# Optimization experiments

Hardware: AMD Instinct MI355X
Metric: run time of the kernel (lower is better)

Reference implementation:

```python
import jax, jax.numpy as jnp
import numpy as np

ENS, N_UNITS, N_HID, IN_DIM, OUT_DIM, BATCH = 10, 256, 7, 6, 201, 16384


def setup_inputs() -> dict:
    key = jax.random.key(0)
    ks = jax.random.split(key, 8)
    # He/fan-in scaled weights so activations stay sane through 8 ReLU layers
    W0 = jax.random.normal(ks[0], (ENS, IN_DIM, N_UNITS), jnp.float32) / np.sqrt(IN_DIM)
    b0 = jax.random.normal(ks[1], (ENS, N_UNITS), jnp.float32) * 0.01
    Wh = jax.random.normal(ks[2], (N_HID, ENS, N_UNITS, N_UNITS), jnp.float32) / np.sqrt(N_UNITS)
    bh = jax.random.normal(ks[3], (N_HID, ENS, N_UNITS), jnp.float32) * 0.01
    Wf = jax.random.normal(ks[4], (ENS, N_UNITS, OUT_DIM), jnp.float32) / np.sqrt(N_UNITS)
    bf = jax.random.normal(ks[5], (ENS, OUT_DIM), jnp.float32) * 0.01
    x = jax.random.normal(ks[6], (BATCH, IN_DIM), jnp.float32)
    return {"x": x, "W0": W0, "b0": b0, "Wh": Wh, "bh": bh, "Wf": Wf, "bf": bf}


def reference(x, W0, b0, Wh, bh, Wf, bf):
    # Ensemble of MLPs (grouped 1x1 conv == per-ensemble dense layers).
    # Input is broadcast to every ensemble member (torch.cat tiling).
    h = jax.nn.relu(jnp.einsum('bi,eio->beo', x, W0) + b0)  # (B, ens, 256)

    def step(h, wb):
        W, b = wb
        return jax.nn.relu(jnp.einsum('beh,eho->beo', h, W) + b), None

    h, _ = jax.lax.scan(step, h, (Wh, bh))  # 7 hidden layers
    y = jnp.einsum('beh,eho->beo', h, Wf) + bf  # (B, ens, out_dim), ens-major channels
    B, E, O = y.shape
    # Faithful to torch: view(B, out_dim, ens_size) on ens-major flat channels,
    # then mean over last dim (mixes strided channel chunks, not true ensemble mean).
    return y.reshape(B, O, E).mean(axis=-1)  # (B, out_dim)
```

## Files before the change

### kernel.cpp

```cpp
#include <hip/hip_runtime.h>

typedef unsigned int u32;
typedef unsigned short ushort_t;

typedef __attribute__((ext_vector_type(8)))  short bf16x8;
typedef __attribute__((ext_vector_type(16))) float f32x16;

#define ENS 10
#define NU 256
#define NHID 7
#define IN_DIM 6
#define OUT_DIM 201
#define BATCH 16384


#define WH_PER 65536
#define WH_TOT (NHID * ENS * WH_PER)
#define W0_PER 4096
#define W0_TOT (ENS * W0_PER)
#define WF_PER 57344
#define WF_TOT (ENS * WF_PER)
#define X_TOT ((BATCH / 32) * 64 * 8)

#define O_WHH 0
#define O_WHL (O_WHH + WH_TOT)
#define O_W0H (O_WHL + WH_TOT)
#define O_W0L (O_W0H + W0_TOT)
#define O_WFH (O_W0L + W0_TOT)
#define O_WFL (O_WFH + WF_TOT)
#define O_XH  (O_WFL + WF_TOT)
#define O_XL  (O_XH + X_TOT)
#define O_P   (O_XL + X_TOT)

#define NG 21
#define RS 264
#define YS 204
#define RT 64

__device__ __forceinline__ u32 bf16_rne(float f) {
    u32 u = __float_as_uint(f);
    return (u + 0x7FFFu + ((u >> 16) & 1u)) >> 16;
}
__device__ __forceinline__ void split2(float f, u32& h, u32& l) {
    h = bf16_rne(f);
    float fh = __uint_as_float(h << 16);
    l = bf16_rne(f - fh);
}

__device__ __forceinline__ u32 cvt_pk_bf16(float s0, float s1) {
    u32 r;
    asm("v_cvt_pk_bf16_f32 %0, %1, %2" : "=v"(r) : "v"(s0), "v"(s1));
    return r;
}

#define GLOAD(dst, p) \
    asm volatile("global_load_dwordx4 %0, %1, off" : "=v"(dst) : "v"(p))
#define VMWAIT4 asm volatile("s_waitcnt vmcnt(4)" ::: "memory")
#define VMWAIT0 asm volatile("s_waitcnt vmcnt(0)" ::: "memory")


__global__ __launch_bounds__(256) void prep_wh(const float* __restrict__ Wh,
                                               ushort_t* __restrict__ dH, ushort_t* __restrict__ dL) {
    int i = blockIdx.x * 256 + threadIdx.x;
    if (i >= WH_TOT) return;
    int j = i & 7, l = (i >> 3) & 63, ctg = (i >> 9) & 7, s = (i >> 12) & 15, le = i >> 16;
    int k = s * 16 + ((l >> 5) << 3) + j;
    int n = ctg * 32 + (l & 31);
    float v = Wh[(size_t)le * 65536 + k * 256 + n];
    u32 h, lo; split2(v, h, lo);
    dH[i] = (ushort_t)h; dL[i] = (ushort_t)lo;
}

__global__ __launch_bounds__(256) void prep_w0(const float* __restrict__ W0,
                                               ushort_t* __restrict__ dH, ushort_t* __restrict__ dL) {
    int i = blockIdx.x * 256 + threadIdx.x;
    if (i >= W0_TOT) return;
    int j = i & 7, l = (i >> 3) & 63, ctg = (i >> 9) & 7, e = i >> 12;
    int k = ((l >> 5) << 3) + j;
    int n = ctg * 32 + (l & 31);
    float v = (k < IN_DIM) ? W0[(e * IN_DIM + k) * 256 + n] : 0.0f;
    u32 h, lo; split2(v, h, lo);
    dH[i] = (ushort_t)h; dL[i] = (ushort_t)lo;
}

__global__ __launch_bounds__(256) void prep_wf(const float* __restrict__ Wf,
                                               ushort_t* __restrict__ dH, ushort_t* __restrict__ dL) {
    int i = blockIdx.x * 256 + threadIdx.x;
    if (i >= WF_TOT) return;
    int e = i / WF_PER;
    int idx = i - e * WF_PER;
    int j = idx & 7, l = (idx >> 3) & 63, g = idx >> 9;
    int s = g / 7, ct = g - s * 7;
    int k = s * 16 + ((l >> 5) << 3) + j;
    int n = ct * 32 + (l & 31);
    float v = (n < OUT_DIM) ? Wf[((size_t)e * 256 + k) * OUT_DIM + n] : 0.0f;
    u32 h, lo; split2(v, h, lo);
    dH[i] = (ushort_t)h; dL[i] = (ushort_t)lo;
}

__global__ __launch_bounds__(256) void prep_x(const float* __restrict__ x,
                                              ushort_t* __restrict__ dH, ushort_t* __restrict__ dL) {
    int i = blockIdx.x * 256 + threadIdx.x;
    if (i >= X_TOT) return;
    int j = i & 7, l = (i >> 3) & 63, rt = i >> 9;
    int row = rt * 32 + (l & 31);
    int k = ((l >> 5) << 3) + j;
    float v = (k < IN_DIM) ? x[row * IN_DIM + k] : 0.0f;
    u32 h, lo; split2(v, h, lo);
    dH[i] = (ushort_t)h; dL[i] = (ushort_t)lo;
}

__global__ __launch_bounds__(256) void reduce_mean(const float* __restrict__ P,
                                                   float* __restrict__ out) {
    int i = blockIdx.x * 256 + threadIdx.x;
    if (i >= BATCH * OUT_DIM) return;
    int b = i / OUT_DIM, jo = i - b * OUT_DIM;
    int f0 = jo * 10;
    int e1 = f0 / OUT_DIM;
    int e2 = (f0 + 9) / OUT_DIM;
    int g1 = jo - (e1 * OUT_DIM) / 10;
    float s = P[((size_t)e1 * BATCH + b) * NG + g1];
    if (e2 != e1) {
        int g2 = jo - (e2 * OUT_DIM) / 10;
        s += P[((size_t)e2 * BATCH + b) * NG + g2];
    }
    out[i] = 0.1f * s;
}

#define MFMA32(A, B, C) __builtin_amdgcn_mfma_f32_32x32x16_bf16((A), (B), (C), 0, 0, 0)

__device__ __forceinline__ void store_act(ushort_t* actH, ushort_t* actL,
    const f32x16 (&acc)[2][2], float bv0, float bv1, int colA, int colB, int rowb)
{
#pragma unroll
    for (int mt = 0; mt < 2; ++mt)
#pragma unroll
        for (int c = 0; c < 2; ++c) {
            const float bv = c ? bv1 : bv0;
            const int col = c ? colB : colA;
#pragma unroll
            for (int q = 0; q < 4; ++q) {
#pragma unroll
                for (int p = 0; p < 2; ++p) {
                    int r0 = q * 4 + p * 2;
                    int row = mt * 32 + rowb + 8 * q + p * 2;
                    float g0 = fmaxf(acc[mt][c][r0] + bv, 0.0f);
                    float g1 = fmaxf(acc[mt][c][r0 + 1] + bv, 0.0f);
                    u32 hp = cvt_pk_bf16(g0, g1);
                    float fh0 = __uint_as_float(hp << 16);
                    float fh1 = __uint_as_float(hp & 0xFFFF0000u);
                    u32 lp = cvt_pk_bf16(g0 - fh0, g1 - fh1);
                    actH[row * RS + col]       = (ushort_t)hp;
                    actH[(row + 1) * RS + col] = (ushort_t)(hp >> 16);
                    actL[row * RS + col]       = (ushort_t)lp;
                    actL[(row + 1) * RS + col] = (ushort_t)(lp >> 16);
                }
            }
        }
}

__global__ __launch_bounds__(256, 2)
void mlp_mfma(const ushort_t* __restrict__ wsU,
              const float* __restrict__ b0g, const float* __restrict__ bhg,
              const float* __restrict__ bfg, float* __restrict__ Pws) {
    __shared__ __align__(16) ushort_t smem[2 * RT * RS];
    ushort_t* actH = smem;
    ushort_t* actL = smem + RT * RS;
    float*    yst  = (float*)smem;

    const int tid  = threadIdx.x;
    const int lane = tid & 63;
    const int cg   = tid >> 6;
    const int l31  = lane & 31;
    const int lh   = lane >> 5;
    const int ctg0 = cg * 2;

    const int bid  = blockIdx.x;
    const int work = (bid & 7) * 320 + (bid >> 3);
    const int e    = work >> 8;
    const int rb   = work & 255;
    const int rowWG = rb * RT;

    const size_t lo8 = (size_t)lane * 8;
    const ushort_t* arH0 = actH + l31 * RS;
    const ushort_t* arL0 = actL + l31 * RS;
    const ushort_t* arH1 = actH + (32 + l31) * RS;
    const ushort_t* arL1 = actL + (32 + l31) * RS;
    const int rowb = lh * 4;
    const int colA = ctg0 * 32 + l31, colB = colA + 32;

    const int c0f = (ctg0 > 6) ? 6 : ctg0;
    const int c1f = (ctg0 + 1 > 6) ? 6 : ctg0 + 1;

    f32x16 acc[2][2];
    bf16x8 aH[2], aL[2];
    bf16x8 sB0h[4], sB0l[4], sB1h[4], sB1l[4];

    {
        const ushort_t* B0H = wsU + O_W0H + (size_t)e * W0_PER;
        const ushort_t* B0L = wsU + O_W0L + (size_t)e * W0_PER;
        bf16x8 b0h0 = *(const bf16x8*)(B0H + (size_t)ctg0 * 512 + lo8);
        bf16x8 b0l0 = *(const bf16x8*)(B0L + (size_t)ctg0 * 512 + lo8);
        bf16x8 b0h1 = *(const bf16x8*)(B0H + (size_t)(ctg0 + 1) * 512 + lo8);
        bf16x8 b0l1 = *(const bf16x8*)(B0L + (size_t)(ctg0 + 1) * 512 + lo8);
        bf16x8 xh[2], xl[2];
#pragma unroll
        for (int mt = 0; mt < 2; ++mt) {
            size_t xoff = ((size_t)(rb * 2 + mt) * 64 + lane) * 8;
            xh[mt] = *(const bf16x8*)(wsU + O_XH + xoff);
            xl[mt] = *(const bf16x8*)(wsU + O_XL + xoff);
        }
        float bv0 = b0g[e * NU + colA];
        float bv1 = b0g[e * NU + colB];

        f32x16 z = 0.0f;
#pragma unroll
        for (int mt = 0; mt < 2; ++mt) {
            f32x16 a0 = z, a1 = z;
            a0 = MFMA32(xh[mt], b0h0, a0);
            a1 = MFMA32(xh[mt], b0h1, a1);
            a0 = MFMA32(xl[mt], b0h0, a0);
            a1 = MFMA32(xl[mt], b0h1, a1);
            a0 = MFMA32(xh[mt], b0l0, a0);
            a1 = MFMA32(xh[mt], b0l1, a1);
            acc[mt][0] = a0; acc[mt][1] = a1;
        }

        VMWAIT0;
        {
            const ushort_t* BH0 = wsU + O_WHH + (size_t)e * WH_PER;
            const ushort_t* BL0 = wsU + O_WHL + (size_t)e * WH_PER;
#pragma unroll
            for (int cc = 0; cc < 2; ++cc) {
                size_t off = ((size_t)(cc * 8 + ctg0)) * 512 + lo8;
                GLOAD(sB0h[cc], BH0 + off);
                GLOAD(sB0l[cc], BL0 + off);
                GLOAD(sB1h[cc], BH0 + off + 512);
                GLOAD(sB1l[cc], BL0 + off + 512);
            }
        }
        store_act(actH, actL, acc, bv0, bv1, colA, colB, rowb);
        __syncthreads();
    }

    const ushort_t* BH = wsU + O_WHH + (size_t)e * WH_PER;
    const ushort_t* BL = wsU + O_WHL + (size_t)e * WH_PER;
#pragma unroll 1
    for (int L = 0; L < NHID; ++L) {
        float bv0 = bhg[(size_t)(L * ENS + e) * NU + colA];
        float bv1 = bhg[(size_t)(L * ENS + e) * NU + colB];

        const ushort_t *nA0[2], *nB0[2], *nA1[2], *nB1[2];
        if (L < NHID - 1) {
            const ushort_t* a_ = BH + (size_t)ENS * WH_PER;
            const ushort_t* b_ = BL + (size_t)ENS * WH_PER;
#pragma unroll
            for (int cc = 0; cc < 2; ++cc) {
                size_t off = ((size_t)(cc * 8 + ctg0)) * 512 + lo8;
                nA0[cc] = a_ + off;       nB0[cc] = b_ + off;
                nA1[cc] = a_ + off + 512; nB1[cc] = b_ + off + 512;
            }
        } else {
            const ushort_t* fh = wsU + O_WFH + (size_t)e * WF_PER;
            const ushort_t* fl = wsU + O_WFL + (size_t)e * WF_PER;
#pragma unroll
            for (int cc = 0; cc < 2; ++cc) {
                size_t o0_ = ((size_t)(cc * 7 + c0f)) * 512 + lo8;
                size_t o1_ = ((size_t)(cc * 7 + c1f)) * 512 + lo8;
                nA0[cc] = fh + o0_; nB0[cc] = fl + o0_;
                nA1[cc] = fh + o1_; nB1[cc] = fl + o1_;
            }
        }

        f32x16 z = 0.0f;
#pragma unroll
        for (int mt = 0; mt < 2; ++mt) { acc[mt][0] = z; acc[mt][1] = z; }
        aH[0] = *(const bf16x8*)(arH0 + lh * 8);
        aL[0] = *(const bf16x8*)(arL0 + lh * 8);
        aH[1] = *(const bf16x8*)(arH1 + lh * 8);
        aL[1] = *(const bf16x8*)(arL1 + lh * 8);

        VMWAIT0;

#pragma unroll
        for (int s = 0; s < 16; ++s) {
            bf16x8 aHn[2], aLn[2];
            if (s < 15) {
                int kn = (s + 1) * 16 + lh * 8;
                aHn[0] = *(const bf16x8*)(arH0 + kn);
                aLn[0] = *(const bf16x8*)(arL0 + kn);
                aHn[1] = *(const bf16x8*)(arH1 + kn);
                aLn[1] = *(const bf16x8*)(arL1 + kn);
            }
            {
                const ushort_t *pA0, *pB0, *pA1, *pB1;
                if (s < 14) {
                    size_t off = ((size_t)((s + 2) * 8 + ctg0)) * 512 + lo8;
                    pA0 = BH + off; pB0 = BL + off;
                    pA1 = BH + off + 512; pB1 = BL + off + 512;
                } else {
                    pA0 = nA0[s - 14]; pB0 = nB0[s - 14];
                    pA1 = nA1[s - 14]; pB1 = nB1[s - 14];
                }
                GLOAD(sB0h[(s + 2) & 3], pA0);
                GLOAD(sB0l[(s + 2) & 3], pB0);
                GLOAD(sB1h[(s + 2) & 3], pA1);
                GLOAD(sB1l[(s + 2) & 3], pB1);
            }
            VMWAIT4;
            __builtin_amdgcn_sched_barrier(0);
#pragma unroll
            for (int mt = 0; mt < 2; ++mt) {
                f32x16 a0 = acc[mt][0], a1 = acc[mt][1];
                a0 = MFMA32(aH[mt], sB0h[s & 3], a0);
                a1 = MFMA32(aH[mt], sB1h[s & 3], a1);
                a0 = MFMA32(aL[mt], sB0h[s & 3], a0);
                a1 = MFMA32(aL[mt], sB1h[s & 3], a1);
                a0 = MFMA32(aH[mt], sB0l[s & 3], a0);
                a1 = MFMA32(aH[mt], sB1l[s & 3], a1);
                acc[mt][0] = a0; acc[mt][1] = a1;
            }
            if (s < 15) {
                aH[0] = aHn[0]; aL[0] = aLn[0];
                aH[1] = aHn[1]; aL[1] = aLn[1];
            }
        }

        __syncthreads();
        store_act(actH, actL, acc, bv0, bv1, colA, colB, rowb);
        __syncthreads();
        BH += (size_t)ENS * WH_PER;
        BL += (size_t)ENS * WH_PER;
    }

    {
        const ushort_t* FH = wsU + O_WFH + (size_t)e * WF_PER;
        const ushort_t* FL = wsU + O_WFL + (size_t)e * WF_PER;
        int o0 = ctg0 * 32 + l31;
        int o1 = (ctg0 + 1) * 32 + l31;
        bool v0 = (o0 < OUT_DIM);
        bool v1 = (ctg0 + 1 < 7) && (o1 < OUT_DIM);
        float bf0 = v0 ? bfg[e * OUT_DIM + o0] : 0.0f;
        float bf1 = v1 ? bfg[e * OUT_DIM + o1] : 0.0f;

        f32x16 z = 0.0f;
#pragma unroll
        for (int mt = 0; mt < 2; ++mt) { acc[mt][0] = z; acc[mt][1] = z; }
        aH[0] = *(const bf16x8*)(arH0 + lh * 8);
        aL[0] = *(const bf16x8*)(arL0 + lh * 8);
        aH[1] = *(const bf16x8*)(arH1 + lh * 8);
        aL[1] = *(const bf16x8*)(arL1 + lh * 8);

        VMWAIT0;

#pragma unroll
        for (int s = 0; s < 16; ++s) {
            bf16x8 aHn[2], aLn[2];
            if (s < 15) {
                int kn = (s + 1) * 16 + lh * 8;
                aHn[0] = *(const bf16x8*)(arH0 + kn);
                aLn[0] = *(const bf16x8*)(arL0 + kn);
                aHn[1] = *(const bf16x8*)(arH1 + kn);
                aLn[1] = *(const bf16x8*)(arL1 + kn);
            }
            if (s < 14) {
                size_t o0_ = ((size_t)((s + 2) * 7 + c0f)) * 512 + lo8;
                size_t o1_ = ((size_t)((s + 2) * 7 + c1f)) * 512 + lo8;
                GLOAD(sB0h[(s + 2) & 3], FH + o0_);
                GLOAD(sB0l[(s + 2) & 3], FL + o0_);
                GLOAD(sB1h[(s + 2) & 3], FH + o1_);
                GLOAD(sB1l[(s + 2) & 3], FL + o1_);
            }
            if (s < 15) { VMWAIT4; } else { VMWAIT0; }
            __builtin_amdgcn_sched_barrier(0);
#pragma unroll
            for (int mt = 0; mt < 2; ++mt) {
                f32x16 a0 = acc[mt][0], a1 = acc[mt][1];
                a0 = MFMA32(aH[mt], sB0h[s & 3], a0);
                a1 = MFMA32(aH[mt], sB1h[s & 3], a1);
                a0 = MFMA32(aL[mt], sB0h[s & 3], a0);
                a1 = MFMA32(aL[mt], sB1h[s & 3], a1);
                a0 = MFMA32(aH[mt], sB0l[s & 3], a0);
                a1 = MFMA32(aH[mt], sB1l[s & 3], a1);
                acc[mt][0] = a0; acc[mt][1] = a1;
            }
            if (s < 15) {
                aH[0] = aHn[0]; aL[0] = aLn[0];
                aH[1] = aHn[1]; aL[1] = aLn[1];
            }
        }

        __syncthreads();
#pragma unroll
        for (int mt = 0; mt < 2; ++mt)
#pragma unroll
            for (int r = 0; r < 16; ++r) {
                int row = mt * 32 + rowb + (r & 3) + 8 * (r >> 2);
                if (v0) yst[row * YS + o0] = acc[mt][0][r] + bf0;
                if (v1) yst[row * YS + o1] = acc[mt][1][r] + bf1;
            }
        __syncthreads();

        const int base_jo = (e * OUT_DIM) / 10;
        const int e201 = e * OUT_DIM;
        for (int it = tid; it < RT * NG; it += 256) {
            int row = it / NG;
            int g   = it - row * NG;
            int f0  = (base_jo + g) * 10;
            float sm = 0.0f;
#pragma unroll
            for (int d = 0; d < 10; ++d) {
                int oo = f0 + d - e201;
                if (oo >= 0 && oo < OUT_DIM) sm += yst[row * YS + oo];
            }
            Pws[((size_t)e * BATCH + rowWG + row) * NG + g] = sm;
        }
    }
}

extern "C" void kernel_launch(void* const* d_in, const int* in_sizes, int n_in,
                              void* d_out, int out_size, void* d_ws, size_t ws_size,
                              hipStream_t stream) {
    const float* x  = (const float*)d_in[0];
    const float* W0 = (const float*)d_in[1];
    const float* b0 = (const float*)d_in[2];
    const float* Wh = (const float*)d_in[3];
    const float* bh = (const float*)d_in[4];
    const float* Wf = (const float*)d_in[5];
    const float* bf = (const float*)d_in[6];
    float* out = (float*)d_out;
    ushort_t* ws = (ushort_t*)d_ws;
    float* Pws = (float*)(ws + O_P);

    prep_wh<<<(WH_TOT + 255) / 256, 256, 0, stream>>>(Wh, ws + O_WHH, ws + O_WHL);
    prep_w0<<<(W0_TOT + 255) / 256, 256, 0, stream>>>(W0, ws + O_W0H, ws + O_W0L);
    prep_wf<<<(WF_TOT + 255) / 256, 256, 0, stream>>>(Wf, ws + O_WFH, ws + O_WFL);
    prep_x <<<(X_TOT  + 255) / 256, 256, 0, stream>>>(x,  ws + O_XH,  ws + O_XL);

    mlp_mfma<<<dim3(BATCH / RT * ENS), 256, 0, stream>>>(ws, b0, bh, bf, Pws);
    reduce_mean<<<(BATCH * OUT_DIM + 255) / 256, 256, 0, stream>>>(Pws, out);
}
```

Measured before the change: 428.7 us.

## Stage biases in LDS and use LDS-only barriers to avoid vmcnt drains

Preloads all hidden and final-layer biases for the ensemble member into shared memory at kernel start. The per-layer bias loads then come from LDS instead of global memory. The __syncthreads calls, which drain outstanding global loads, become an lgkmcnt-only wait plus s_barrier, and the explicit vmcnt(0) waits before each layer's K loop are removed. Weight prefetches can therefore stay in flight across barriers. The risk is correctness: the loop relies on the per-step vmcnt waits being enough for prefetched weights, and the LDS preload is ordered only by the first LDS barrier.

```diff
diff --git a/kernel.cpp b/kernel.cpp
--- a/kernel.cpp
+++ b/kernel.cpp
@@ -57,6 +57,8 @@
     asm volatile("global_load_dwordx4 %0, %1, off" : "=v"(dst) : "v"(p))
 #define VMWAIT4 asm volatile("s_waitcnt vmcnt(4)" ::: "memory")
 #define VMWAIT0 asm volatile("s_waitcnt vmcnt(0)" ::: "memory")
+#define LBAR() do { asm volatile("s_waitcnt lgkmcnt(0)" ::: "memory"); \
+                    __builtin_amdgcn_s_barrier(); } while (0)
 
 
 __global__ __launch_bounds__(256) void prep_wh(const float* __restrict__ Wh,
@@ -167,6 +169,7 @@
     ushort_t* actH = smem;
     ushort_t* actL = smem + RT * RS;
     float*    yst  = (float*)smem;
+    __shared__ float biasLds[NHID * NU + 224];
 
     const int tid  = threadIdx.x;
     const int lane = tid & 63;
@@ -195,6 +198,15 @@
     f32x16 acc[2][2];
     bf16x8 aH[2], aL[2];
     bf16x8 sB0h[4], sB0l[4], sB1h[4], sB1l[4];
+
+#pragma unroll
+    for (int it = 0; it < NHID; ++it) {
+        int i = it * 256 + tid;
+        int L = i >> 8, c = i & 255;
+        biasLds[i] = bhg[(size_t)(L * ENS + e) * NU + c];
+    }
+    if (tid < 224)
+        biasLds[NHID * NU + tid] = (tid < OUT_DIM) ? bfg[e * OUT_DIM + tid] : 0.0f;
 
     {
         const ushort_t* B0H = wsU + O_W0H + (size_t)e * W0_PER;
@@ -240,15 +252,15 @@
             }
         }
         store_act(actH, actL, acc, bv0, bv1, colA, colB, rowb);
-        __syncthreads();
+        LBAR();
     }
 
     const ushort_t* BH = wsU + O_WHH + (size_t)e * WH_PER;
     const ushort_t* BL = wsU + O_WHL + (size_t)e * WH_PER;
 #pragma unroll 1
     for (int L = 0; L < NHID; ++L) {
-        float bv0 = bhg[(size_t)(L * ENS + e) * NU + colA];
-        float bv1 = bhg[(size_t)(L * ENS + e) * NU + colB];
+        float bv0 = biasLds[L * NU + colA];
+        float bv1 = biasLds[L * NU + colB];
 
         const ushort_t *nA0[2], *nB0[2], *nA1[2], *nB1[2];
         if (L < NHID - 1) {
@@ -279,8 +291,6 @@
         aL[0] = *(const bf16x8*)(arL0 + lh * 8);
         aH[1] = *(const bf16x8*)(arH1 + lh * 8);
         aL[1] = *(const bf16x8*)(arL1 + lh * 8);
-
-        VMWAIT0;
 
 #pragma unroll
         for (int s = 0; s < 16; ++s) {
@@ -326,9 +336,9 @@
             }
         }
 
-        __syncthreads();
+        LBAR();
         store_act(actH, actL, acc, bv0, bv1, colA, colB, rowb);
-        __syncthreads();
+        LBAR();
         BH += (size_t)ENS * WH_PER;
         BL += (size_t)ENS * WH_PER;
     }
@@ -340,8 +350,8 @@
         int o1 = (ctg0 + 1) * 32 + l31;
         bool v0 = (o0 < OUT_DIM);
         bool v1 = (ctg0 + 1 < 7) && (o1 < OUT_DIM);
-        float bf0 = v0 ? bfg[e * OUT_DIM + o0] : 0.0f;
-        float bf1 = v1 ? bfg[e * OUT_DIM + o1] : 0.0f;
+        float bf0 = v0 ? biasLds[NHID * NU + o0] : 0.0f;
+        float bf1 = v1 ? biasLds[NHID * NU + o1] : 0.0f;
 
         f32x16 z = 0.0f;
 #pragma unroll
@@ -350,8 +360,6 @@
         aL[0] = *(const bf16x8*)(arL0 + lh * 8);
         aH[1] = *(const bf16x8*)(arH1 + lh * 8);
         aL[1] = *(const bf16x8*)(arL1 + lh * 8);
-
-        VMWAIT0;
 
 #pragma unroll
         for (int s = 0; s < 16; ++s) {
@@ -390,7 +398,7 @@
             }
         }
 
-        __syncthreads();
+        LBAR();
 #pragma unroll
         for (int mt = 0; mt < 2; ++mt)
 #pragma unroll
@@ -399,7 +407,7 @@
                 if (v0) yst[row * YS + o0] = acc[mt][0][r] + bf0;
                 if (v1) yst[row * YS + o1] = acc[mt][1][r] + bf1;
             }
-        __syncthreads();
+        LBAR();
 
         const int base_jo = (e * OUT_DIM) / 10;
         const int e201 = e * OUT_DIM;
```

Result: no change. 427.9 us (-0.2%).
